# Optimization experiments

Measured on AMD Instinct MI355X. Metric: run time of the kernel, lower is better.

The kernel has to match this reference:

```python
import jax, jax.numpy as jnp
import numpy as np

N_NODES = 100000


def gcn_conv(x, edge_index, W, b, n):
    # PyG GCNConv: add self-loops, symmetric normalization, then scatter-add.
    src, dst = edge_index[0], edge_index[1]
    loop = jnp.arange(n, dtype=src.dtype)
    src = jnp.concatenate([src, loop])
    dst = jnp.concatenate([dst, loop])
    h = x @ W  # [n, out]
    deg = jnp.zeros((n,), dtype=x.dtype).at[dst].add(1.0)
    dinv = jnp.where(deg > 0, jax.lax.rsqrt(deg), 0.0)
    norm = dinv[src] * dinv[dst]  # [E+n]
    msg = h[src] * norm[:, None]  # gather + scale
    out = jax.ops.segment_sum(msg, dst, num_segments=n)  # scatter-add
    return out + b


def setup_inputs() -> dict:
    key = jax.random.key(0)
    ks = jax.random.split(key, 6)
    n, f, h, c, e = N_NODES, 128, 32, 7, 3200000
    x = jax.random.normal(ks[0], (n, f), dtype=jnp.float32)
    edge_index = jax.random.randint(ks[1], (2, e), 0, n, dtype=jnp.int64)
    W1 = jax.random.normal(ks[2], (f, h), dtype=jnp.float32) * (1.0 / np.sqrt(f))
    b1 = jnp.zeros((h,), dtype=jnp.float32)
    W2 = jax.random.normal(ks[3], (h, c), dtype=jnp.float32) * (1.0 / np.sqrt(h))
    b2 = jnp.zeros((c,), dtype=jnp.float32)
    return {"x": x, "edge_index": edge_index, "W1": W1, "b1": b1, "W2": W2, "b2": b2}


def reference(x, edge_index, W1, b1, W2, b2):
    n = x.shape[0]
    h = jax.nn.relu(gcn_conv(x, edge_index, W1, b1, n))
    # F.dropout(training=False) is identity in eval mode
    out = gcn_conv(h, edge_index, W2, b2, n)
    return jax.nn.log_softmax(out, axis=1)
```

## Files before the change

### kernel.cpp

```cpp
#include <hip/hip_runtime.h>
#include <math.h>


#define F_IN   128
#define F_HID  32
#define F_OUT  7
#define TILE   8192
#define BSH    8
#define BNODES 256
#define HSZ    512
#define PCAP   10240
#define QSH    13
#define NQ     16

typedef __attribute__((ext_vector_type(8))) short bf16x8;
typedef __attribute__((ext_vector_type(4))) float f32x4;
typedef __attribute__((ext_vector_type(4))) int   i32x4;

__device__ __forceinline__ float bf2f(unsigned short u) {
    return __uint_as_float(((unsigned int)u) << 16);
}
__device__ __forceinline__ unsigned short f2bf(float f) {
    unsigned int u = __float_as_uint(f);
    u += 0x7FFF + ((u >> 16) & 1);
    return (unsigned short)(u >> 16);
}
__device__ __forceinline__ unsigned int pack2(unsigned short lo, unsigned short hi) {
    return (unsigned int)lo | ((unsigned int)hi << 16);
}
#define NTL(p) __builtin_nontemporal_load(p)

__device__ __forceinline__ void acc8(float* a, uint4 v) {
    a[0] += bf2f((unsigned short)v.x); a[1] += bf2f((unsigned short)(v.x >> 16));
    a[2] += bf2f((unsigned short)v.y); a[3] += bf2f((unsigned short)(v.y >> 16));
    a[4] += bf2f((unsigned short)v.z); a[5] += bf2f((unsigned short)(v.z >> 16));
    a[6] += bf2f((unsigned short)v.w); a[7] += bf2f((unsigned short)(v.w >> 16));
}

__global__ __launch_bounds__(512)
void k_histGemm(const int* __restrict__ dst, int E, int NB, int NT,
                int* __restrict__ counts,
                const float* __restrict__ x, const float* __restrict__ W1,
                unsigned short* __restrict__ g1b, int n) {
    int t = threadIdx.x;
    if (blockIdx.x < (unsigned)NT) {
        __shared__ int h[HSZ];
        int tile = blockIdx.x;
        for (int i = t; i < NB; i += 512) h[i] = 0;
        __syncthreads();
        int base = tile * TILE;
        int lim = base + TILE; if (lim > E) lim = E;
        int n4 = (lim - base) >> 2;
        const i32x4* d4 = (const i32x4*)(dst + base);
        for (int i = t; i < n4; i += 512) {
            i32x4 d = NTL(&d4[i]);
            atomicAdd(&h[d[0] >> BSH], 1);
            atomicAdd(&h[d[1] >> BSH], 1);
            atomicAdd(&h[d[2] >> BSH], 1);
            atomicAdd(&h[d[3] >> BSH], 1);
        }
        __syncthreads();
        for (int i = t; i < NB; i += 512) counts[tile * NB + i] = h[i];
        return;
    }
    int gb = blockIdx.x - NT;
    int wave = t >> 6;
    int lane = t & 63;
    int row0 = (gb * 8 + wave) * 16;
    if (row0 >= n) return;
    bf16x8 bfr[2][4];
    #pragma unroll
    for (int nt = 0; nt < 2; ++nt)
        #pragma unroll
        for (int ks = 0; ks < 4; ++ks) {
            bf16x8 w;
            #pragma unroll
            for (int j = 0; j < 8; ++j) {
                int k = ks * 32 + ((lane >> 4) << 3) + j;
                w[j] = (short)f2bf(W1[k * F_HID + nt * 16 + (lane & 15)]);
            }
            bfr[nt][ks] = w;
        }
    int arow = row0 + (lane & 15);
    const float* xr = x + (size_t)arow * F_IN + ((lane >> 4) << 3);
    f32x4 acc0 = {0.f, 0.f, 0.f, 0.f};
    f32x4 acc1 = {0.f, 0.f, 0.f, 0.f};
    #pragma unroll
    for (int ks = 0; ks < 4; ++ks) {
        f32x4 lo = NTL((const f32x4*)(xr + ks * 32));
        f32x4 hi = NTL((const f32x4*)(xr + ks * 32 + 4));
        bf16x8 a;
        a[0] = (short)f2bf(lo[0]); a[1] = (short)f2bf(lo[1]);
        a[2] = (short)f2bf(lo[2]); a[3] = (short)f2bf(lo[3]);
        a[4] = (short)f2bf(hi[0]); a[5] = (short)f2bf(hi[1]);
        a[6] = (short)f2bf(hi[2]); a[7] = (short)f2bf(hi[3]);
        acc0 = __builtin_amdgcn_mfma_f32_16x16x32_bf16(a, bfr[0][ks], acc0, 0, 0, 0);
        acc1 = __builtin_amdgcn_mfma_f32_16x16x32_bf16(a, bfr[1][ks], acc1, 0, 0, 0);
    }
    int col = lane & 15;
    #pragma unroll
    for (int rr = 0; rr < 4; ++rr) {
        int orow = row0 + ((lane >> 4) << 2) + rr;
        g1b[(size_t)orow * F_HID + col]      = f2bf(acc0[rr]);
        g1b[(size_t)orow * F_HID + col + 16] = f2bf(acc1[rr]);
    }
}

__global__ void k_scanLocal(const int* __restrict__ counts, int NSCAN, int NB, int NT,
                            int* __restrict__ tileOffset, int* __restrict__ bsum) {
    __shared__ int s[1024];
    int t = threadIdx.x;
    int idx = blockIdx.x * 1024 + t;
    int v = 0;
    if (idx < NSCAN) { int b = idx / NT, tt = idx - b * NT; v = counts[tt * NB + b]; }
    s[t] = v;
    __syncthreads();
    for (int off = 1; off < 1024; off <<= 1) {
        int a = (t >= off) ? s[t - off] : 0;
        __syncthreads();
        s[t] += a;
        __syncthreads();
    }
    if (idx < NSCAN) tileOffset[idx] = s[t] - v;
    if (t == 1023) bsum[blockIdx.x] = s[1023];
}

__global__ void k_scanAdd(int* __restrict__ tileOffset, int NSCAN,
                          const int* __restrict__ bsum, int nsb) {
    __shared__ int s[1024];
    int t = threadIdx.x;
    int blk = blockIdx.x;
    s[t] = (t < blk && t < nsb) ? bsum[t] : 0;
    __syncthreads();
    for (int off = 512; off > 0; off >>= 1) {
        if (t < off) s[t] += s[t + off];
        __syncthreads();
    }
    int offv = s[0];
    int idx = blk * 1024 + t;
    if (idx < NSCAN) tileOffset[idx] += offv;
}

__global__ __launch_bounds__(512)
void k_tileFill(const int* __restrict__ src, const int* __restrict__ dst,
                int E, int NB, int NT, const int* __restrict__ tileOffset,
                int* __restrict__ pairBuf) {
    __shared__ int lcur[HSZ];
    int bid = blockIdx.x;
    int xcd = bid & 7;
    int idx = bid >> 3;
    int q = NT >> 3, r = NT & 7;
    int tile = (xcd < r ? xcd * (q + 1) : r * (q + 1) + (xcd - r) * q) + idx;
    int t = threadIdx.x;
    for (int i = t; i < NB; i += 512) lcur[i] = tileOffset[i * NT + tile];
    __syncthreads();
    int base = tile * TILE;
    int lim = base + TILE; if (lim > E) lim = E;
    int n4 = (lim - base) >> 2;
    const i32x4* s4 = (const i32x4*)(src + base);
    const i32x4* d4 = (const i32x4*)(dst + base);
    for (int i = t; i < n4; i += 512) {
        i32x4 s = NTL(&s4[i]);
        i32x4 d = NTL(&d4[i]);
        #pragma unroll
        for (int k = 0; k < 4; ++k) {
            int b = d[k] >> BSH;
            int pos = atomicAdd(&lcur[b], 1);
            pairBuf[pos] = ((d[k] & (BNODES - 1)) << 17) | s[k];
        }
    }
}

__global__ __launch_bounds__(512)
void k_bucketCSR(const int* __restrict__ pairBuf, const int* __restrict__ tileOffset,
                 int NT, int NB, int E, int n,
                 int* __restrict__ degi, int* __restrict__ cursor,
                 float* __restrict__ dinv, int* __restrict__ srcSorted,
                 uint4* __restrict__ g1q) {
    __shared__ int outb[PCAP];
    __shared__ int cntq[BNODES * NQ];
    __shared__ int pref[BNODES * NQ];
    __shared__ int sred[512];
    __shared__ float sdinv[BNODES];
    int b = blockIdx.x, t = threadIdx.x;
    for (int i = t; i < BNODES * NQ; i += 512) cntq[i] = 0;
    __syncthreads();
    int bs = tileOffset[b * NT];
    int be = (b + 1 < NB) ? tileOffset[(b + 1) * NT] : E;
    int sz = be - bs;
    for (int j = bs + t; j < be; j += 512) {
        int p = pairBuf[j];
        int idx = ((p >> 17) << 4) | ((p >> QSH) & (NQ - 1));
        atomicAdd(&cntq[idx], 1);
    }
    __syncthreads();
    int loc[8];
    int base8 = t << 3;
    int sum = 0;
    #pragma unroll
    for (int k = 0; k < 8; ++k) { loc[k] = cntq[base8 + k]; sum += loc[k]; }
    sred[t] = sum;
    __syncthreads();
    for (int off = 1; off < 512; off <<= 1) {
        int a = (t >= off) ? sred[t - off] : 0;
        __syncthreads();
        sred[t] += a;
        __syncthreads();
    }
    int run = sred[t] - sum;
    #pragma unroll
    for (int k = 0; k < 8; ++k) { pref[base8 + k] = run; run += loc[k]; }
    __syncthreads();
    if (t < BNODES) {
        int node = (b << BSH) + t;
        if (node < n) {
            int dsum = 0;
            #pragma unroll
            for (int k = 0; k < NQ; ++k) dsum += cntq[(t << 4) + k];
            float di = rsqrtf((float)dsum + 1.0f);
            degi[node]   = dsum;
            cursor[node] = bs + pref[t << 4];
            dinv[node]   = di;
            sdinv[t]     = di;
        }
    }
    __syncthreads();
    for (int j = bs + t; j < be; j += 512) {
        int p = pairBuf[j];
        int idx = ((p >> 17) << 4) | ((p >> QSH) & (NQ - 1));
        int pos = atomicAdd(&pref[idx], 1);
        int s = p & 0x1FFFF;
        if (pos < PCAP) outb[pos] = s;
        else            srcSorted[bs + pos] = s;
    }
    __syncthreads();
    int lim = sz < PCAP ? sz : PCAP;
    for (int idx = t; idx < lim; idx += 512) srcSorted[bs + idx] = outb[idx];
    int nodeBase = b << BSH;
    for (int i = t; i < BNODES * 4; i += 512) {
        int node = nodeBase + (i >> 2);
        if (node < n) {
            float di = sdinv[i >> 2];
            uint4 v = g1q[(size_t)node * 4 + (i & 3)];
            uint4 o;
            o.x = pack2(f2bf(di * bf2f((unsigned short)v.x)),
                        f2bf(di * bf2f((unsigned short)(v.x >> 16))));
            o.y = pack2(f2bf(di * bf2f((unsigned short)v.y)),
                        f2bf(di * bf2f((unsigned short)(v.y >> 16))));
            o.z = pack2(f2bf(di * bf2f((unsigned short)v.z)),
                        f2bf(di * bf2f((unsigned short)(v.z >> 16))));
            o.w = pack2(f2bf(di * bf2f((unsigned short)v.w)),
                        f2bf(di * bf2f((unsigned short)(v.w >> 16))));
            g1q[(size_t)node * 4 + (i & 3)] = o;
        }
    }
}

__global__ void k_gather1l2(const uint4* __restrict__ g1q, const int* __restrict__ srcSorted,
                            const int* __restrict__ cursor, const int* __restrict__ degi,
                            const float* __restrict__ dinv, const float* __restrict__ b1,
                            const float* __restrict__ W2, uint4* __restrict__ g2q, int n) {
    int t = threadIdx.x;
    int c = t & 7;
    int q = c >> 2;
    int f = c & 3;
    int node = blockIdx.x * 32 + (t >> 3);
    if (node >= n) return;
    int start = cursor[node];
    int end = start + degi[node];
    float a[8], b[8];
    #pragma unroll
    for (int k = 0; k < 8; ++k) { a[k] = 0.f; b[k] = 0.f; }
    if (q == 0) acc8(a, g1q[node * 4 + f]);
    int j = start + q;
    for (; j + 6 < end; j += 8) {
        int s0 = srcSorted[j];
        int s1 = srcSorted[j + 2];
        int s2 = srcSorted[j + 4];
        int s3 = srcSorted[j + 6];
        uint4 v0 = g1q[s0 * 4 + f];
        uint4 v1 = g1q[s1 * 4 + f];
        uint4 v2 = g1q[s2 * 4 + f];
        uint4 v3 = g1q[s3 * 4 + f];
        acc8(a, v0); acc8(b, v1); acc8(a, v2); acc8(b, v3);
    }
    for (; j < end; j += 2) acc8(a, g1q[srcSorted[j] * 4 + f]);
    float af[8];
    #pragma unroll
    for (int k = 0; k < 8; ++k) {
        af[k] = a[k] + b[k];
        af[k] += __shfl_xor(af[k], 4, 64);
    }
    float di = dinv[node];
    float h[8];
    #pragma unroll
    for (int k = 0; k < 8; ++k) {
        float v = di * af[k] + b1[8 * f + k];
        h[k] = v > 0.f ? v : 0.f;
    }
    float p[F_OUT];
    #pragma unroll
    for (int k = 0; k < F_OUT; ++k) {
        float s = 0.f;
        #pragma unroll
        for (int f8 = 0; f8 < 8; ++f8) s += h[f8] * W2[(8 * f + f8) * F_OUT + k];
        p[k] = s;
    }
    #pragma unroll
    for (int m = 1; m < 4; m <<= 1) {
        #pragma unroll
        for (int k = 0; k < F_OUT; ++k) p[k] += __shfl_xor(p[k], m, 64);
    }
    if (c == 0) {
        uint4 qv;
        qv.x = pack2(f2bf(di * p[0]), f2bf(di * p[1]));
        qv.y = pack2(f2bf(di * p[2]), f2bf(di * p[3]));
        qv.z = pack2(f2bf(di * p[4]), f2bf(di * p[5]));
        qv.w = pack2(f2bf(di * p[6]), 0);
        g2q[node] = qv;
    }
}

__global__ void k_gather2final(const uint4* __restrict__ g2q,
                               const int* __restrict__ srcSorted,
                               const int* __restrict__ cursor, const int* __restrict__ degi,
                               const float* __restrict__ dinv, const float* __restrict__ b2,
                               float* __restrict__ out, int n) {
    int node = blockIdx.x * 256 + threadIdx.x;
    if (node >= n) return;
    int start = cursor[node];
    int end = start + degi[node];
    float A[8], B[8];
    #pragma unroll
    for (int f = 0; f < 8; ++f) { A[f] = 0.f; B[f] = 0.f; }
    acc8(A, g2q[node]);
    int j = start;
    while (j < end && (j & 3)) { acc8(B, g2q[srcSorted[j]]); ++j; }
    for (; j + 4 <= end; j += 4) {
        i32x4 sA = *(const i32x4*)&srcSorted[j];
        uint4 r0 = g2q[sA[0]];
        uint4 r1 = g2q[sA[1]];
        uint4 r2 = g2q[sA[2]];
        uint4 r3 = g2q[sA[3]];
        acc8(A, r0); acc8(B, r1); acc8(A, r2); acc8(B, r3);
    }
    for (; j < end; ++j) acc8(A, g2q[srcSorted[j]]);
    float di = dinv[node];
    float v[F_OUT];
    float m = -1e30f;
    #pragma unroll
    for (int k = 0; k < F_OUT; ++k) {
        v[k] = di * (A[k] + B[k]) + b2[k];
        m = fmaxf(m, v[k]);
    }
    float ssum = 0.f;
    #pragma unroll
    for (int k = 0; k < F_OUT; ++k) ssum += __expf(v[k] - m);
    float ls = __logf(ssum) + m;
    #pragma unroll
    for (int k = 0; k < F_OUT; ++k)
        __builtin_nontemporal_store(v[k] - ls, &out[node * F_OUT + k]);
}

extern "C" void kernel_launch(void* const* d_in, const int* in_sizes, int n_in,
                              void* d_out, int out_size, void* d_ws, size_t ws_size,
                              hipStream_t stream) {
    const float* x  = (const float*)d_in[0];
    const int*   ei = (const int*)d_in[1];
    const float* W1 = (const float*)d_in[2];
    const float* b1 = (const float*)d_in[3];
    const float* W2 = (const float*)d_in[4];
    const float* b2 = (const float*)d_in[5];
    float* out = (float*)d_out;

    int n = in_sizes[0] / F_IN;
    int E = in_sizes[1] / 2;
    const int* src = ei;
    const int* dst = ei + E;
    int NB = (n + BNODES - 1) >> BSH;
    int NT = (E + TILE - 1) / TILE;
    int NSCAN = NB * NT;
    int nsb = (NSCAN + 1023) / 1024;
    int ngem = (n + 127) / 128;

    int*            degi       = (int*)d_ws;
    int*            cursor     = degi + n;
    float*          dinv       = (float*)(cursor + n);
    int*            srcSorted  = (int*)(dinv + n);
    int*            pairBuf    = srcSorted + E;
    unsigned short* g1b        = (unsigned short*)(pairBuf + E);
    unsigned short* g2b        = g1b + (size_t)n * F_HID;
    int*            counts     = (int*)(g2b + (size_t)n * 8);
    int*            tileOffset = counts + NSCAN;
    int*            bsum       = tileOffset + NSCAN;

    k_histGemm<<<NT + ngem, 512, 0, stream>>>(dst, E, NB, NT, counts, x, W1, g1b, n);
    k_scanLocal<<<nsb, 1024, 0, stream>>>(counts, NSCAN, NB, NT, tileOffset, bsum);
    k_scanAdd<<<nsb, 1024, 0, stream>>>(tileOffset, NSCAN, bsum, nsb);
    k_tileFill<<<NT, 512, 0, stream>>>(src, dst, E, NB, NT, tileOffset, pairBuf);
    k_bucketCSR<<<NB, 512, 0, stream>>>(pairBuf, tileOffset, NT, NB, E, n,
                                        degi, cursor, dinv, srcSorted, (uint4*)g1b);
    k_gather1l2<<<(n + 31) / 32, 256, 0, stream>>>((const uint4*)g1b, srcSorted, cursor, degi,
                                                   dinv, b1, W2, (uint4*)g2b, n);
    k_gather2final<<<(n + 255) / 256, 256, 0, stream>>>((const uint4*)g2b, srcSorted, cursor,
                                                        degi, dinv, b2, out, n);
}
```

Measured before the change: 140.4 us.

## Fold scan block-sum add into consumers and shrink per-node sub-buckets to four

Removes the k_scanAdd launch. k_tileFill and k_bucketCSR now each compute a prefix of the scan block sums in shared memory and add it when they read tileOffset. In k_bucketCSR, the per-node sub-bucketing changes from 16 bins keyed on source bits to 4 bins keyed on source-range thresholds. This cuts shared histogram size and shrinks the prefix scan from 512 to 256 threads. The trade-off is a redundant 512-entry scan in every block, which caps nsb at 512, plus coarser source ordering within each node.

Result: no change. 140.7 us (+0.2%).

```diff
diff --git a/kernel.cpp b/kernel.cpp
--- a/kernel.cpp
+++ b/kernel.cpp
@@ -10,8 +10,6 @@
 #define BNODES 256
 #define HSZ    512
 #define PCAP   10240
-#define QSH    13
-#define NQ     16
 
 typedef __attribute__((ext_vector_type(8))) short bf16x8;
 typedef __attribute__((ext_vector_type(4))) float f32x4;
@@ -125,34 +123,40 @@
     if (t == 1023) bsum[blockIdx.x] = s[1023];
 }
 
-__global__ void k_scanAdd(int* __restrict__ tileOffset, int NSCAN,
-                          const int* __restrict__ bsum, int nsb) {
-    __shared__ int s[1024];
-    int t = threadIdx.x;
-    int blk = blockIdx.x;
-    s[t] = (t < blk && t < nsb) ? bsum[t] : 0;
-    __syncthreads();
-    for (int off = 512; off > 0; off >>= 1) {
-        if (t < off) s[t] += s[t + off];
-        __syncthreads();
-    }
-    int offv = s[0];
-    int idx = blk * 1024 + t;
-    if (idx < NSCAN) tileOffset[idx] += offv;
+__device__ __forceinline__ void bsumPrefix(const int* __restrict__ bsum, int nsb,
+                                           int* sbp, int t, int nthreads) {
+    if (t < 512) sbp[t] = (t < nsb) ? bsum[t] : 0;
+    __syncthreads();
+    for (int off = 1; off < 512; off <<= 1) {
+        int a = 0;
+        if (t < 512 && t >= off) a = sbp[t - off];
+        __syncthreads();
+        if (t < 512) sbp[t] += a;
+        __syncthreads();
+    }
+}
+__device__ __forceinline__ int sbpEx(const int* sbp, int k) {
+    return k ? sbp[k - 1] : 0;
 }
 
 __global__ __launch_bounds__(512)
 void k_tileFill(const int* __restrict__ src, const int* __restrict__ dst,
                 int E, int NB, int NT, const int* __restrict__ tileOffset,
+                const int* __restrict__ bsum, int nsb,
                 int* __restrict__ pairBuf) {
     __shared__ int lcur[HSZ];
+    __shared__ int sbp[512];
     int bid = blockIdx.x;
     int xcd = bid & 7;
     int idx = bid >> 3;
     int q = NT >> 3, r = NT & 7;
     int tile = (xcd < r ? xcd * (q + 1) : r * (q + 1) + (xcd - r) * q) + idx;
     int t = threadIdx.x;
-    for (int i = t; i < NB; i += 512) lcur[i] = tileOffset[i * NT + tile];
+    bsumPrefix(bsum, nsb, sbp, t, 512);
+    for (int i = t; i < NB; i += 512) {
+        int gi = i * NT + tile;
+        lcur[i] = tileOffset[gi] + sbpEx(sbp, gi >> 10);
+    }
     __syncthreads();
     int base = tile * TILE;
     int lim = base + TILE; if (lim > E) lim = E;
@@ -173,53 +177,62 @@
 
 __global__ __launch_bounds__(512)
 void k_bucketCSR(const int* __restrict__ pairBuf, const int* __restrict__ tileOffset,
+                 const int* __restrict__ bsum, int nsb,
                  int NT, int NB, int E, int n,
                  int* __restrict__ degi, int* __restrict__ cursor,
                  float* __restrict__ dinv, int* __restrict__ srcSorted,
                  uint4* __restrict__ g1q) {
     __shared__ int outb[PCAP];
-    __shared__ int cntq[BNODES * NQ];
-    __shared__ int pref[BNODES * NQ];
-    __shared__ int sred[512];
+    __shared__ int cntq[BNODES * 4];
+    __shared__ int pref[BNODES * 4];
+    __shared__ int sred[BNODES];
+    __shared__ int sbp[512];
     __shared__ float sdinv[BNODES];
     int b = blockIdx.x, t = threadIdx.x;
-    for (int i = t; i < BNODES * NQ; i += 512) cntq[i] = 0;
-    __syncthreads();
-    int bs = tileOffset[b * NT];
-    int be = (b + 1 < NB) ? tileOffset[(b + 1) * NT] : E;
+    bsumPrefix(bsum, nsb, sbp, t, 512);
+    for (int i = t; i < BNODES * 4; i += 512) cntq[i] = 0;
+    __syncthreads();
+    int gi0 = b * NT;
+    int bs = tileOffset[gi0] + sbpEx(sbp, gi0 >> 10);
+    int be;
+    if (b + 1 < NB) {
+        int gi1 = (b + 1) * NT;
+        be = tileOffset[gi1] + sbpEx(sbp, gi1 >> 10);
+    } else be = E;
     int sz = be - bs;
+    int th1 = n >> 2, th2 = n >> 1, th3 = (n >> 2) + (n >> 1);
     for (int j = bs + t; j < be; j += 512) {
         int p = pairBuf[j];
-        int idx = ((p >> 17) << 4) | ((p >> QSH) & (NQ - 1));
-        atomicAdd(&cntq[idx], 1);
-    }
-    __syncthreads();
-    int loc[8];
-    int base8 = t << 3;
-    int sum = 0;
-    #pragma unroll
-    for (int k = 0; k < 8; ++k) { loc[k] = cntq[base8 + k]; sum += loc[k]; }
-    sred[t] = sum;
-    __syncthreads();
-    for (int off = 1; off < 512; off <<= 1) {
-        int a = (t >= off) ? sred[t - off] : 0;
-        __syncthreads();
-        sred[t] += a;
-        __syncthreads();
-    }
-    int run = sred[t] - sum;
-    #pragma unroll
-    for (int k = 0; k < 8; ++k) { pref[base8 + k] = run; run += loc[k]; }
-    __syncthreads();
+        int s = p & 0x1FFFF;
+        int q = (s >= th1) + (s >= th2) + (s >= th3);
+        atomicAdd(&cntq[((p >> 17) << 2) | q], 1);
+    }
+    __syncthreads();
+    int v0 = 0, v1 = 0, v2 = 0, v3 = 0, sum = 0, base = 0;
     if (t < BNODES) {
+        base = t << 2;
+        v0 = cntq[base]; v1 = cntq[base + 1]; v2 = cntq[base + 2]; v3 = cntq[base + 3];
+        sum = v0 + v1 + v2 + v3;
+        sred[t] = sum;
+    }
+    __syncthreads();
+    for (int off = 1; off < BNODES; off <<= 1) {
+        int a = (t < BNODES && t >= off) ? sred[t - off] : 0;
+        __syncthreads();
+        if (t < BNODES) sred[t] += a;
+        __syncthreads();
+    }
+    if (t < BNODES) {
+        int ex = sred[t] - sum;
+        pref[base]     = ex;
+        pref[base + 1] = ex + v0;
+        pref[base + 2] = ex + v0 + v1;
+        pref[base + 3] = ex + v0 + v1 + v2;
         int node = (b << BSH) + t;
         if (node < n) {
-            int dsum = 0;
-            #pragma unroll
-            for (int k = 0; k < NQ; ++k) dsum += cntq[(t << 4) + k];
-            float di = rsqrtf((float)dsum + 1.0f);
-            degi[node]   = dsum;
-            cursor[node] = bs + pref[t << 4];
+            float di = rsqrtf((float)sum + 1.0f);
+            degi[node]   = sum;
+            cursor[node] = bs + ex;
             dinv[node]   = di;
             sdinv[t]     = di;
         }
@@ -227,9 +240,9 @@
     __syncthreads();
     for (int j = bs + t; j < be; j += 512) {
         int p = pairBuf[j];
-        int idx = ((p >> 17) << 4) | ((p >> QSH) & (NQ - 1));
-        int pos = atomicAdd(&pref[idx], 1);
         int s = p & 0x1FFFF;
+        int q = (s >= th1) + (s >= th2) + (s >= th3);
+        int pos = atomicAdd(&pref[((p >> 17) << 2) | q], 1);
         if (pos < PCAP) outb[pos] = s;
         else            srcSorted[bs + pos] = s;
     }
@@ -396,9 +409,8 @@
 
     k_histGemm<<<NT + ngem, 512, 0, stream>>>(dst, E, NB, NT, counts, x, W1, g1b, n);
     k_scanLocal<<<nsb, 1024, 0, stream>>>(counts, NSCAN, NB, NT, tileOffset, bsum);
-    k_scanAdd<<<nsb, 1024, 0, stream>>>(tileOffset, NSCAN, bsum, nsb);
-    k_tileFill<<<NT, 512, 0, stream>>>(src, dst, E, NB, NT, tileOffset, pairBuf);
-    k_bucketCSR<<<NB, 512, 0, stream>>>(pairBuf, tileOffset, NT, NB, E, n,
+    k_tileFill<<<NT, 512, 0, stream>>>(src, dst, E, NB, NT, tileOffset, bsum, nsb, pairBuf);
+    k_bucketCSR<<<NB, 512, 0, stream>>>(pairBuf, tileOffset, bsum, nsb, NT, NB, E, n,
                                         degi, cursor, dinv, srcSorted, (uint4*)g1b);
     k_gather1l2<<<(n + 31) / 32, 256, 0, stream>>>((const uint4*)g1b, srcSorted, cursor, degi,
                                                    dinv, b1, W2, (uint4*)g2b, n);
```
